# Optimization experiments

Hardware: AMD Instinct MI355X
Metric: run time of the kernel (lower is better)

The kernel has to match this reference:

```python
import jax, jax.numpy as jnp
import numpy as np

B = 256
C = 16      # data_channels
H = 256     # hidden_channels
P = 2       # prop_layers
T = 1000    # predict_length


def setup_inputs() -> dict:
    key = jax.random.key(0)
    ks = jax.random.split(key, 7)
    return {
        "y0": jax.random.normal(ks[0], (B, C), jnp.float32),
        "in_weight": jax.random.normal(ks[1], (B, C, H), jnp.float32),
        "in_bias": jax.random.normal(ks[2], (B, H), jnp.float32),
        "out_weight": jax.random.normal(ks[3], (B, H, C), jnp.float32),
        "out_bias": jax.random.normal(ks[4], (B, C), jnp.float32),
        "prop_weight": jax.random.normal(ks[5], (B, P, H, H), jnp.float32),
        "prop_bias": jax.random.normal(ks[6], (B, P, H), jnp.float32),
        "cutoff": jnp.ones((1,), jnp.float32),
        "predict_length": T,
    }


def reference(y0, in_weight, in_bias, out_weight, out_bias,
              prop_weight, prop_bias, cutoff, predict_length):
    dt = 1e-6
    n_prop = prop_weight.shape[1]

    def f(y):  # y: [B, C]
        h = jax.nn.relu(jnp.einsum('bc,bch->bh', y, in_weight) + in_bias)
        for j in range(n_prop):  # small fixed layer count
            h = jax.nn.relu(jnp.einsum('bh,bhk->bk', h, prop_weight[:, j]) + prop_bias[:, j])
        return jnp.einsum('bh,bhc->bc', h, out_weight) + out_bias

    def step(y, _):
        y = y + cutoff * jnp.tanh(dt * f(y) / cutoff)
        return y, y

    _, ys = jax.lax.scan(step, y0, None, length=predict_length)  # [T, B, C]
    return jnp.transpose(ys, (1, 2, 0))  # [B, C, T]
```

## Files before the change

### kernel.cpp

```cpp
#include <hip/hip_runtime.h>
#include <cstddef>

#define HD 256
#define CD 16
#define BLOCK 256

struct alignas(16) SMem {
  float w0[128 * HD];
  float win[CD * HD];
  float part[4][HD];
  float h[HD];
  float outp[BLOCK];
  float bin[HD];
  float b0[HD];
  float b1[HD];
  float y[CD];
  float bout[CD];
};

__global__ __launch_bounds__(BLOCK, 1)
void decoder_persistent(const float* __restrict__ y0,
                        const float* __restrict__ in_w,
                        const float* __restrict__ in_b,
                        const float* __restrict__ out_w,
                        const float* __restrict__ out_b,
                        const float* __restrict__ prop_w,
                        const float* __restrict__ prop_b,
                        const float* __restrict__ cutoff,
                        const int*   __restrict__ plen,
                        float* __restrict__ out)
{
  __shared__ SMem sm;
  const int b  = blockIdx.x;
  const int t  = threadIdx.x;
  const int e  = t >> 6;
  const int cg = t & 63;
  const int T  = plen[0];
  const float ct = cutoff[0];
  const float dtc = 1e-6f;

  const float* W0g = prop_w + (size_t)b * 2u * HD * HD;
  const float* W1g = W0g + HD * HD;
  const float* Wig = in_w  + (size_t)b * CD * HD;
  const float* Wog = out_w + (size_t)b * HD * CD;

  for (int idx = t; idx < 128 * HD / 4; idx += BLOCK) {
    const int L  = idx >> 6;
    const int q  = idx & 63;
    const int gr = ((L >> 5) * 64) + (L & 31);
    *(float4*)(sm.w0 + L * HD + q * 4) =
        *(const float4*)(W0g + (size_t)gr * HD + q * 4);
  }
  for (int idx = t; idx < CD * HD / 4; idx += BLOCK) {
    *(float4*)(sm.win + idx * 4) = *(const float4*)(Wig + idx * 4);
  }
  sm.bin[t] = in_b[(size_t)b * HD + t];
  sm.b0[t]  = prop_b[((size_t)b * 2) * HD + t];
  sm.b1[t]  = prop_b[((size_t)b * 2 + 1) * HD + t];
  if (t < CD) {
    sm.bout[t] = out_b[(size_t)b * CD + t];
    sm.y[t]    = y0[(size_t)b * CD + t];
  }

  float w0r[32][4];
#pragma unroll
  for (int j = 0; j < 32; ++j) {
    const float4 v = *(const float4*)(W0g + (size_t)(e * 64 + 32 + j) * HD + cg * 4);
    w0r[j][0] = v.x; w0r[j][1] = v.y; w0r[j][2] = v.z; w0r[j][3] = v.w;
  }
  float w1r[64][4];
#pragma unroll
  for (int j = 0; j < 64; ++j) {
    const float4 v = *(const float4*)(W1g + (size_t)(e * 64 + j) * HD + cg * 4);
    w1r[j][0] = v.x; w1r[j][1] = v.y; w1r[j][2] = v.z; w1r[j][3] = v.w;
  }
  const int oc = t & 15;
  const int og = t >> 4;
  float wor[16];
#pragma unroll
  for (int j = 0; j < 16; ++j) wor[j] = Wog[(size_t)(og * 16 + j) * CD + oc];

  __syncthreads();

  float* outb = out + (size_t)b * CD * T;
  const int rbase = e * 64;
  const int lb    = e * 32;

  for (int step = 0; step < T; ++step) {
    {
      float ax = 0.f, ay = 0.f, az = 0.f, aw = 0.f;
#pragma unroll
      for (int c2 = 0; c2 < 4; ++c2) {
        const float yv = sm.y[e * 4 + c2];
        const float4 w = *(const float4*)(sm.win + (e * 4 + c2) * HD + cg * 4);
        ax += yv * w.x; ay += yv * w.y; az += yv * w.z; aw += yv * w.w;
      }
      float4 a; a.x = ax; a.y = ay; a.z = az; a.w = aw;
      *(float4*)(&sm.part[e][cg * 4]) = a;
    }
    __syncthreads();
    {
      float s = sm.bin[t] + sm.part[0][t] + sm.part[1][t] + sm.part[2][t] + sm.part[3][t];
      sm.h[t] = fmaxf(s, 0.0f);
    }
    __syncthreads();
    {
      float ax = 0.f, ay = 0.f, az = 0.f, aw = 0.f;
#pragma unroll
      for (int rc = 0; rc < 8; ++rc) {
        const float4 hv = *(const float4*)(sm.h + rbase + rc * 4);
        const float4 wa = *(const float4*)(sm.w0 + (lb + rc * 4 + 0) * HD + cg * 4);
        const float4 wb = *(const float4*)(sm.w0 + (lb + rc * 4 + 1) * HD + cg * 4);
        const float4 wc = *(const float4*)(sm.w0 + (lb + rc * 4 + 2) * HD + cg * 4);
        const float4 wd = *(const float4*)(sm.w0 + (lb + rc * 4 + 3) * HD + cg * 4);
        ax += hv.x * wa.x + hv.y * wb.x + hv.z * wc.x + hv.w * wd.x;
        ay += hv.x * wa.y + hv.y * wb.y + hv.z * wc.y + hv.w * wd.y;
        az += hv.x * wa.z + hv.y * wb.z + hv.z * wc.z + hv.w * wd.z;
        aw += hv.x * wa.w + hv.y * wb.w + hv.z * wc.w + hv.w * wd.w;
      }
#pragma unroll
      for (int rc = 0; rc < 8; ++rc) {
        const float4 hv = *(const float4*)(sm.h + rbase + 32 + rc * 4);
        ax += hv.x*w0r[rc*4+0][0] + hv.y*w0r[rc*4+1][0] + hv.z*w0r[rc*4+2][0] + hv.w*w0r[rc*4+3][0];
        ay += hv.x*w0r[rc*4+0][1] + hv.y*w0r[rc*4+1][1] + hv.z*w0r[rc*4+2][1] + hv.w*w0r[rc*4+3][1];
        az += hv.x*w0r[rc*4+0][2] + hv.y*w0r[rc*4+1][2] + hv.z*w0r[rc*4+2][2] + hv.w*w0r[rc*4+3][2];
        aw += hv.x*w0r[rc*4+0][3] + hv.y*w0r[rc*4+1][3] + hv.z*w0r[rc*4+2][3] + hv.w*w0r[rc*4+3][3];
      }
      float4 a; a.x = ax; a.y = ay; a.z = az; a.w = aw;
      *(float4*)(&sm.part[e][cg * 4]) = a;
    }
    __syncthreads();
    {
      float s = sm.b0[t] + sm.part[0][t] + sm.part[1][t] + sm.part[2][t] + sm.part[3][t];
      sm.h[t] = fmaxf(s, 0.0f);
    }
    __syncthreads();
    {
      float ax = 0.f, ay = 0.f, az = 0.f, aw = 0.f;
#pragma unroll
      for (int rc = 0; rc < 16; ++rc) {
        const float4 hv = *(const float4*)(sm.h + rbase + rc * 4);
        ax += hv.x*w1r[rc*4+0][0] + hv.y*w1r[rc*4+1][0] + hv.z*w1r[rc*4+2][0] + hv.w*w1r[rc*4+3][0];
        ay += hv.x*w1r[rc*4+0][1] + hv.y*w1r[rc*4+1][1] + hv.z*w1r[rc*4+2][1] + hv.w*w1r[rc*4+3][1];
        az += hv.x*w1r[rc*4+0][2] + hv.y*w1r[rc*4+1][2] + hv.z*w1r[rc*4+2][2] + hv.w*w1r[rc*4+3][2];
        aw += hv.x*w1r[rc*4+0][3] + hv.y*w1r[rc*4+1][3] + hv.z*w1r[rc*4+2][3] + hv.w*w1r[rc*4+3][3];
      }
      float4 a; a.x = ax; a.y = ay; a.z = az; a.w = aw;
      *(float4*)(&sm.part[e][cg * 4]) = a;
    }
    __syncthreads();
    {
      float s = sm.b1[t] + sm.part[0][t] + sm.part[1][t] + sm.part[2][t] + sm.part[3][t];
      sm.h[t] = fmaxf(s, 0.0f);
    }
    __syncthreads();
    {
      float acc = 0.f;
#pragma unroll
      for (int j = 0; j < 16; ++j) acc += sm.h[og * 16 + j] * wor[j];
      sm.outp[t] = acc;
    }
    __syncthreads();
    if (t < CD) {
      float s = sm.bout[t];
#pragma unroll
      for (int g = 0; g < 16; ++g) s += sm.outp[t + g * 16];
      const float yv = sm.y[t] + ct * tanhf(dtc * s / ct);
      sm.y[t] = yv;
      outb[(size_t)t * T + step] = yv;
    }
    __syncthreads();
  }
}

extern "C" void kernel_launch(void* const* d_in, const int* in_sizes, int n_in,
                              void* d_out, int out_size, void* d_ws, size_t ws_size,
                              hipStream_t stream) {
  (void)in_sizes; (void)n_in; (void)out_size; (void)d_ws; (void)ws_size;
  const float* y0     = (const float*)d_in[0];
  const float* in_w   = (const float*)d_in[1];
  const float* in_b   = (const float*)d_in[2];
  const float* out_w  = (const float*)d_in[3];
  const float* out_b  = (const float*)d_in[4];
  const float* prop_w = (const float*)d_in[5];
  const float* prop_b = (const float*)d_in[6];
  const float* cutoff = (const float*)d_in[7];
  const int*   plen   = (const int*)d_in[8];
  float* out = (float*)d_out;

  decoder_persistent<<<256, BLOCK, 0, stream>>>(
      y0, in_w, in_b, out_w, out_b, prop_w, prop_b, cutoff, plen, out);
}
```

Baseline: 3.895 ms.

## Give each thread a full output column to drop cross-wave partial reductions and barriers

The work split changes so each thread owns one hidden output column and computes the full dot product over all 256 inputs. This removes the four-way partial-sum buffers and the extra reduction phases, cutting per-step barriers from eight to four. The first prop layer now holds 144 weight rows in registers and 112 rows in LDS, layer two is fully in registers, and the input and output layers use register weights with shuffles. The y state is replicated per thread in registers instead of shared memory. Each thread now needs over 400 weight registers, which risks spills, and every thread reads all of h from LDS as broadcasts.

```diff
diff --git a/kernel.cpp b/kernel.cpp
--- a/kernel.cpp
+++ b/kernel.cpp
@@ -4,18 +4,15 @@
 #define HD 256
 #define CD 16
 #define BLOCK 256
+#define W0REG 144
+#define W0LDS 112
 
 struct alignas(16) SMem {
-  float w0[128 * HD];
-  float win[CD * HD];
-  float part[4][HD];
-  float h[HD];
-  float outp[BLOCK];
-  float bin[HD];
-  float b0[HD];
-  float b1[HD];
-  float y[CD];
-  float bout[CD];
+  float w0L[W0LDS * HD];
+  float hA[HD];
+  float hB[HD];
+  float hC[HD];
+  float op[4][CD];
 };
 
 __global__ __launch_bounds__(BLOCK, 1)
@@ -33,10 +30,12 @@
   __shared__ SMem sm;
   const int b  = blockIdx.x;
   const int t  = threadIdx.x;
+  const int l  = t & 63;
   const int e  = t >> 6;
-  const int cg = t & 63;
+  const int oc = l & 15;
+  const int og = l >> 4;
   const int T  = plen[0];
-  const float ct = cutoff[0];
+  const float ct  = cutoff[0];
   const float dtc = 1e-6f;
 
   const float* W0g = prop_w + (size_t)b * 2u * HD * HD;
@@ -44,132 +43,120 @@
   const float* Wig = in_w  + (size_t)b * CD * HD;
   const float* Wog = out_w + (size_t)b * HD * CD;
 
-  for (int idx = t; idx < 128 * HD / 4; idx += BLOCK) {
-    const int L  = idx >> 6;
-    const int q  = idx & 63;
-    const int gr = ((L >> 5) * 64) + (L & 31);
-    *(float4*)(sm.w0 + L * HD + q * 4) =
-        *(const float4*)(W0g + (size_t)gr * HD + q * 4);
+  float winr[CD];
+#pragma unroll
+  for (int c = 0; c < CD; ++c) winr[c] = Wig[c * HD + t];
+
+  float w0r[W0REG];
+#pragma unroll
+  for (int r = 0; r < W0REG; ++r) w0r[r] = W0g[(size_t)r * HD + t];
+
+  float w1r[HD];
+#pragma unroll
+  for (int r = 0; r < HD; ++r) w1r[r] = W1g[(size_t)r * HD + t];
+
+  float woutr[16];
+#pragma unroll
+  for (int j = 0; j < 16; ++j) woutr[j] = Wog[(size_t)(e * 64 + og * 16 + j) * CD + oc];
+
+  const float binr  = in_b[(size_t)b * HD + t];
+  const float b0r   = prop_b[((size_t)b * 2) * HD + t];
+  const float b1r   = prop_b[((size_t)b * 2 + 1) * HD + t];
+  const float boutr = out_b[(size_t)b * CD + oc];
+  float ymine = y0[(size_t)b * CD + oc];
+
+  for (int i = t; i < W0LDS * (HD / 4); i += BLOCK) {
+    const int L = i >> 6;
+    const int q = i & 63;
+    *(float4*)(sm.w0L + L * HD + q * 4) =
+        *(const float4*)(W0g + (size_t)(W0REG + L) * HD + q * 4);
   }
-  for (int idx = t; idx < CD * HD / 4; idx += BLOCK) {
-    *(float4*)(sm.win + idx * 4) = *(const float4*)(Wig + idx * 4);
-  }
-  sm.bin[t] = in_b[(size_t)b * HD + t];
-  sm.b0[t]  = prop_b[((size_t)b * 2) * HD + t];
-  sm.b1[t]  = prop_b[((size_t)b * 2 + 1) * HD + t];
-  if (t < CD) {
-    sm.bout[t] = out_b[(size_t)b * CD + t];
-    sm.y[t]    = y0[(size_t)b * CD + t];
-  }
-
-  float w0r[32][4];
-#pragma unroll
-  for (int j = 0; j < 32; ++j) {
-    const float4 v = *(const float4*)(W0g + (size_t)(e * 64 + 32 + j) * HD + cg * 4);
-    w0r[j][0] = v.x; w0r[j][1] = v.y; w0r[j][2] = v.z; w0r[j][3] = v.w;
-  }
-  float w1r[64][4];
-#pragma unroll
-  for (int j = 0; j < 64; ++j) {
-    const float4 v = *(const float4*)(W1g + (size_t)(e * 64 + j) * HD + cg * 4);
-    w1r[j][0] = v.x; w1r[j][1] = v.y; w1r[j][2] = v.z; w1r[j][3] = v.w;
-  }
-  const int oc = t & 15;
-  const int og = t >> 4;
-  float wor[16];
-#pragma unroll
-  for (int j = 0; j < 16; ++j) wor[j] = Wog[(size_t)(og * 16 + j) * CD + oc];
-
   __syncthreads();
 
+  const float* w0La = sm.w0L + t;
+  const float* w0Lb = sm.w0L + 64 * HD + t;
+
   float* outb = out + (size_t)b * CD * T;
-  const int rbase = e * 64;
-  const int lb    = e * 32;
 
   for (int step = 0; step < T; ++step) {
     {
-      float ax = 0.f, ay = 0.f, az = 0.f, aw = 0.f;
+      float acc = binr;
 #pragma unroll
-      for (int c2 = 0; c2 < 4; ++c2) {
-        const float yv = sm.y[e * 4 + c2];
-        const float4 w = *(const float4*)(sm.win + (e * 4 + c2) * HD + cg * 4);
-        ax += yv * w.x; ay += yv * w.y; az += yv * w.z; aw += yv * w.w;
+      for (int c = 0; c < CD; ++c) {
+        const float yc = __shfl(ymine, (l & 48) + c);
+        acc = fmaf(yc, winr[c], acc);
       }
-      float4 a; a.x = ax; a.y = ay; a.z = az; a.w = aw;
-      *(float4*)(&sm.part[e][cg * 4]) = a;
+      sm.hA[t] = fmaxf(acc, 0.0f);
     }
     __syncthreads();
+
     {
-      float s = sm.bin[t] + sm.part[0][t] + sm.part[1][t] + sm.part[2][t] + sm.part[3][t];
-      sm.h[t] = fmaxf(s, 0.0f);
+      float a0 = b0r, a1 = 0.f, a2 = 0.f, a3 = 0.f;
+#pragma unroll
+      for (int rq = 0; rq < W0REG / 4; ++rq) {
+        const float4 hv = *(const float4*)(sm.hA + rq * 4);
+        a0 = fmaf(hv.x, w0r[rq * 4 + 0], a0);
+        a1 = fmaf(hv.y, w0r[rq * 4 + 1], a1);
+        a2 = fmaf(hv.z, w0r[rq * 4 + 2], a2);
+        a3 = fmaf(hv.w, w0r[rq * 4 + 3], a3);
+      }
+#pragma unroll
+      for (int rq = 0; rq < 16; ++rq) {
+        const float4 hv = *(const float4*)(sm.hA + W0REG + rq * 4);
+        a0 = fmaf(hv.x, w0La[(rq * 4 + 0) * HD], a0);
+        a1 = fmaf(hv.y, w0La[(rq * 4 + 1) * HD], a1);
+        a2 = fmaf(hv.z, w0La[(rq * 4 + 2) * HD], a2);
+        a3 = fmaf(hv.w, w0La[(rq * 4 + 3) * HD], a3);
+      }
+#pragma unroll
+      for (int rq = 0; rq < 12; ++rq) {
+        const float4 hv = *(const float4*)(sm.hA + W0REG + 64 + rq * 4);
+        a0 = fmaf(hv.x, w0Lb[(rq * 4 + 0) * HD], a0);
+        a1 = fmaf(hv.y, w0Lb[(rq * 4 + 1) * HD], a1);
+        a2 = fmaf(hv.z, w0Lb[(rq * 4 + 2) * HD], a2);
+        a3 = fmaf(hv.w, w0Lb[(rq * 4 + 3) * HD], a3);
+      }
+      sm.hB[t] = fmaxf((a0 + a1) + (a2 + a3), 0.0f);
     }
     __syncthreads();
+
     {
-      float ax = 0.f, ay = 0.f, az = 0.f, aw = 0.f;
+      float c0 = b1r, c1 = 0.f, c2 = 0.f, c3 = 0.f;
 #pragma unroll
-      for (int rc = 0; rc < 8; ++rc) {
-        const float4 hv = *(const float4*)(sm.h + rbase + rc * 4);
-        const float4 wa = *(const float4*)(sm.w0 + (lb + rc * 4 + 0) * HD + cg * 4);
-        const float4 wb = *(const float4*)(sm.w0 + (lb + rc * 4 + 1) * HD + cg * 4);
-        const float4 wc = *(const float4*)(sm.w0 + (lb + rc * 4 + 2) * HD + cg * 4);
-        const float4 wd = *(const float4*)(sm.w0 + (lb + rc * 4 + 3) * HD + cg * 4);
-        ax += hv.x * wa.x + hv.y * wb.x + hv.z * wc.x + hv.w * wd.x;
-        ay += hv.x * wa.y + hv.y * wb.y + hv.z * wc.y + hv.w * wd.y;
-        az += hv.x * wa.z + hv.y * wb.z + hv.z * wc.z + hv.w * wd.z;
-        aw += hv.x * wa.w + hv.y * wb.w + hv.z * wc.w + hv.w * wd.w;
+      for (int rq = 0; rq < HD / 4; ++rq) {
+        const float4 hv = *(const float4*)(sm.hB + rq * 4);
+        c0 = fmaf(hv.x, w1r[rq * 4 + 0], c0);
+        c1 = fmaf(hv.y, w1r[rq * 4 + 1], c1);
+        c2 = fmaf(hv.z, w1r[rq * 4 + 2], c2);
+        c3 = fmaf(hv.w, w1r[rq * 4 + 3], c3);
       }
-#pragma unroll
-      for (int rc = 0; rc < 8; ++rc) {
-        const float4 hv = *(const float4*)(sm.h + rbase + 32 + rc * 4);
-        ax += hv.x*w0r[rc*4+0][0] + hv.y*w0r[rc*4+1][0] + hv.z*w0r[rc*4+2][0] + hv.w*w0r[rc*4+3][0];
-        ay += hv.x*w0r[rc*4+0][1] + hv.y*w0r[rc*4+1][1] + hv.z*w0r[rc*4+2][1] + hv.w*w0r[rc*4+3][1];
-        az += hv.x*w0r[rc*4+0][2] + hv.y*w0r[rc*4+1][2] + hv.z*w0r[rc*4+2][2] + hv.w*w0r[rc*4+3][2];
-        aw += hv.x*w0r[rc*4+0][3] + hv.y*w0r[rc*4+1][3] + hv.z*w0r[rc*4+2][3] + hv.w*w0r[rc*4+3][3];
-      }
-      float4 a; a.x = ax; a.y = ay; a.z = az; a.w = aw;
-      *(float4*)(&sm.part[e][cg * 4]) = a;
+      sm.hC[t] = fmaxf((c0 + c1) + (c2 + c3), 0.0f);
     }
     __syncthreads();
+
     {
-      float s = sm.b0[t] + sm.part[0][t] + sm.part[1][t] + sm.part[2][t] + sm.part[3][t];
-      sm.h[t] = fmaxf(s, 0.0f);
+      float p = 0.f;
+#pragma unroll
+      for (int jq = 0; jq < 4; ++jq) {
+        const float4 hv = *(const float4*)(sm.hC + e * 64 + og * 16 + jq * 4);
+        p = fmaf(hv.x, woutr[jq * 4 + 0], p);
+        p = fmaf(hv.y, woutr[jq * 4 + 1], p);
+        p = fmaf(hv.z, woutr[jq * 4 + 2], p);
+        p = fmaf(hv.w, woutr[jq * 4 + 3], p);
+      }
+      p += __shfl_xor(p, 16);
+      p += __shfl_xor(p, 32);
+      if (l < CD) sm.op[e][l] = p;
     }
     __syncthreads();
+
     {
-      float ax = 0.f, ay = 0.f, az = 0.f, aw = 0.f;
-#pragma unroll
-      for (int rc = 0; rc < 16; ++rc) {
-        const float4 hv = *(const float4*)(sm.h + rbase + rc * 4);
-        ax += hv.x*w1r[rc*4+0][0] + hv.y*w1r[rc*4+1][0] + hv.z*w1r[rc*4+2][0] + hv.w*w1r[rc*4+3][0];
-        ay += hv.x*w1r[rc*4+0][1] + hv.y*w1r[rc*4+1][1] + hv.z*w1r[rc*4+2][1] + hv.w*w1r[rc*4+3][1];
-        az += hv.x*w1r[rc*4+0][2] + hv.y*w1r[rc*4+1][2] + hv.z*w1r[rc*4+2][2] + hv.w*w1r[rc*4+3][2];
-        aw += hv.x*w1r[rc*4+0][3] + hv.y*w1r[rc*4+1][3] + hv.z*w1r[rc*4+2][3] + hv.w*w1r[rc*4+3][3];
-      }
-      float4 a; a.x = ax; a.y = ay; a.z = az; a.w = aw;
-      *(float4*)(&sm.part[e][cg * 4]) = a;
+      const float s  = boutr + ((sm.op[0][oc] + sm.op[1][oc]) +
+                                (sm.op[2][oc] + sm.op[3][oc]));
+      const float yv = ymine + ct * tanhf(dtc * s / ct);
+      ymine = yv;
+      if (t < CD) outb[(size_t)t * T + step] = yv;
     }
-    __syncthreads();
-    {
-      float s = sm.b1[t] + sm.part[0][t] + sm.part[1][t] + sm.part[2][t] + sm.part[3][t];
-      sm.h[t] = fmaxf(s, 0.0f);
-    }
-    __syncthreads();
-    {
-      float acc = 0.f;
-#pragma unroll
-      for (int j = 0; j < 16; ++j) acc += sm.h[og * 16 + j] * wor[j];
-      sm.outp[t] = acc;
-    }
-    __syncthreads();
-    if (t < CD) {
-      float s = sm.bout[t];
-#pragma unroll
-      for (int g = 0; g < 16; ++g) s += sm.outp[t + g * 16];
-      const float yv = sm.y[t] + ct * tanhf(dtc * s / ct);
-      sm.y[t] = yv;
-      outb[(size_t)t * T + step] = yv;
-    }
-    __syncthreads();
   }
 }
 
```

After: 6.916 ms. 1.78x slower.
